# Kernel optimization log

Measured on AMD Instinct MI355X. Metric: run time of the kernel, lower is better.

The kernel has to match this reference:

```python
import jax, jax.numpy as jnp
import numpy as np

N, C, T, V, E = 4, 64, 64, 1024, 4096
IN_CH, OUT_CH, H = 256, 512, 8
DH = OUT_CH // H


def _leaky(x):
    return jnp.where(x >= 0, x, 0.01 * x)


def _mlp(x, w1, b1, w2, b2, g, b):
    # Linear -> LeakyReLU -> (dropout: eval identity) -> Linear -> BatchNorm(batch stats) -> LeakyReLU
    h = _leaky(x @ w1 + b1)
    h = h @ w2 + b2
    n, e, f = h.shape
    flat = h.reshape(n * e, f)
    mu = flat.mean(0)
    var = flat.var(0)  # biased variance, as torch BatchNorm uses for normalization
    flat = (flat - mu) * jax.lax.rsqrt(var + 1e-5) * g + b
    return _leaky(flat.reshape(n, e, f))


def _attn(q, k, v, wq, bq, wk, bk, wv, bv, wf, bf):
    # SelfAttention with scale=1: embed dim == OUT_CH, H heads of DH dims
    n, lq, _ = q.shape
    def split(t):
        return t.reshape(n, -1, H, DH).transpose(0, 2, 1, 3)  # (n, H, L, DH)
    Q = split(q @ wq + bq)
    K = split(k @ wk + bk)
    Vv = split(v @ wv + bv)
    scale = jnp.sqrt(jnp.float32(DH))
    att = jax.nn.softmax(jnp.einsum("nhqd,nhkd->nhqk", Q, K) / scale, axis=-1)
    x = jnp.einsum("nhqk,nhkd->nhqd", att, Vv)
    x = x.transpose(0, 2, 1, 3).reshape(n, lq, OUT_CH)
    return x @ wf + bf


def setup_inputs():
    key = jax.random.key(0)
    ks = list(jax.random.split(key, 24))

    def lin(k1, n_in, n_out):
        w = jax.random.normal(k1, (n_in, n_out), jnp.float32) * np.sqrt(2.0 / (n_in + n_out))
        b = jnp.full((n_out,), 0.1, jnp.float32)
        return w, b

    inp = {
        "x1": jax.random.normal(ks[0], (N, C, T, V), jnp.float32),
        "x2": jax.random.normal(ks[1], (N, C, T, V), jnp.float32),
        "encode1": jax.random.uniform(ks[2], (E, V), dtype=jnp.float32),
        "encode2": jax.random.uniform(ks[3], (E, V), dtype=jnp.float32),
    }
    i = 4
    for name in ("mlp", "nlp"):
        inp[name + "_w1"], inp[name + "_b1"] = lin(ks[i], 2 * IN_CH, OUT_CH); i += 1
        inp[name + "_w2"], inp[name + "_b2"] = lin(ks[i], OUT_CH, OUT_CH); i += 1
        inp[name + "_gamma"] = jnp.ones((OUT_CH,), jnp.float32)
        inp[name + "_beta"] = jnp.zeros((OUT_CH,), jnp.float32)
    for name in ("att1", "att2"):
        for p in ("wq", "wk", "wv", "fc"):
            inp[name + "_" + p + "_w"], inp[name + "_" + p + "_b"] = lin(ks[i], OUT_CH, OUT_CH); i += 1
    return inp


def reference(x1, x2, encode1, encode2,
              mlp_w1, mlp_b1, mlp_w2, mlp_b2, mlp_gamma, mlp_beta,
              nlp_w1, nlp_b1, nlp_w2, nlp_b2, nlp_gamma, nlp_beta,
              att1_wq_w, att1_wq_b, att1_wk_w, att1_wk_b, att1_wv_w, att1_wv_b, att1_fc_w, att1_fc_b,
              att2_wq_w, att2_wq_b, att2_wk_w, att2_wk_b, att2_wv_w, att2_wv_b, att2_fc_w, att2_fc_b):
    n, c, t, v = x1.shape

    def prep(x):
        # permute(0,2,3,1).view(N,V,-1) then AdaptiveAvgPool1d(IN_CH) with exact windows
        x = jnp.transpose(x, (0, 2, 3, 1)).reshape(n, v, t * c)
        return x.reshape(n, v, IN_CH, (t * c) // IN_CH).mean(-1)

    x1p = prep(x1)
    x2p = prep(x2)

    def node_enc(x):
        return jnp.concatenate([
            jnp.einsum("ev,nvc->nec", encode1, x),
            jnp.einsum("ev,nvc->nec", encode2, x),
        ], axis=-1)  # (N, E, 2*IN_CH)

    h1 = _mlp(node_enc(x1p), mlp_w1, mlp_b1, mlp_w2, mlp_b2, mlp_gamma, mlp_beta)
    h2 = _mlp(node_enc(x2p), nlp_w1, nlp_b1, nlp_w2, nlp_b2, nlp_gamma, nlp_beta)

    def edge_enc(h):
        r = jnp.einsum("ev,nec->nvc", encode1, h)  # (N, V, OUT_CH)
        return r / r.shape[1]

    e1 = edge_enc(h1)
    e2 = edge_enc(h2)

    a1 = _attn(e2, e1, e1, att1_wq_w, att1_wq_b, att1_wk_w, att1_wk_b, att1_wv_w, att1_wv_b, att1_fc_w, att1_fc_b)
    a2 = _attn(e1, e2, e2, att2_wq_w, att2_wq_b, att2_wk_w, att2_wk_b, att2_wv_w, att2_wv_b, att2_fc_w, att2_fc_b)

    c1 = jnp.concatenate([a1, a2], axis=1)  # (N, 2V, OUT_CH)
    c2 = jnp.concatenate([a2, a1], axis=1)
    A = jax.nn.softmax(jnp.einsum("nic,njc->nij", c1, c2), axis=-1)  # (N, 2V, 2V)
    # normalize_dynamic_digraph: AGCN-style column-degree normalization A @ D^{-1}
    col = A.sum(axis=1, keepdims=True)
    return A * jnp.where(col > 0, 1.0 / col, 0.0)
```

## Files before the change

### kernel.cpp

```cpp
#include <hip/hip_runtime.h>
#include <hip/hip_bf16.h>

#define LEAKY(v) ((v) >= 0.f ? (v) : 0.01f * (v))

typedef __attribute__((ext_vector_type(8))) short short8b;
typedef __attribute__((ext_vector_type(4))) float f32x4;
typedef __attribute__((ext_vector_type(4))) unsigned short us4;

__device__ __forceinline__ unsigned short f2b(float f) {
  unsigned int u = __builtin_bit_cast(unsigned int, f);
  return (unsigned short)((u + 0x7FFFu + ((u >> 16) & 1u)) >> 16);
}
__device__ __forceinline__ float b2f(unsigned short s) {
  return __builtin_bit_cast(float, (unsigned int)s << 16);
}

__device__ __forceinline__ void gload16(const unsigned short* g, unsigned short* l) {
  __builtin_amdgcn_global_load_lds(
      (const __attribute__((address_space(1))) unsigned int*)(g),
      (__attribute__((address_space(3))) unsigned int*)(l), 16, 0, 0);
}

__device__ __forceinline__ void stage64(const unsigned short* g, int ldg,
                                        unsigned short* lds, int lane, int w) {
  const int r8 = lane >> 3;
  const int ce = ((lane & 7) ^ r8) << 3;
  const int r0 = w * 8 + r8;
  gload16(g + (long)r0 * ldg + ce, lds + w * 512);
  gload16(g + (long)(r0 + 32) * ldg + ce, lds + 2048 + w * 512);
}

__device__ __forceinline__ short8b ldsw(const unsigned short* base, int row, int c4) {
  return *(const short8b*)&base[row * 64 + (((c4 ^ (row & 7)) << 3))];
}

__global__ __launch_bounds__(256) void prep_pool(const float* __restrict__ X1,
                                                 const float* __restrict__ X2,
                                                 unsigned short* __restrict__ P) {
  const float* X = blockIdx.z ? X2 : X1;
  unsigned short* Pb = P + (long)blockIdx.z * (1L << 20);
  const int i = blockIdx.x, n = blockIdx.y;
  const int t = i >> 4;
  const int vvb = (i & 15) * 64;
  __shared__ float tile[64][65];
  const int tid = threadIdx.x;
  const long base = (((long)n * 64) * 64 + t) * 1024 + vvb;
#pragma unroll
  for (int it = 0; it < 16; ++it) {
    int idx = tid + it * 256;
    int c = idx >> 6, w = idx & 63;
    tile[c][w] = X[base + (long)c * 64 * 1024 + w];
  }
  __syncthreads();
  const int k = tid;
  const int w = k >> 2, cb = (k & 3) * 16;
  float s = 0.f;
#pragma unroll
  for (int m = 0; m < 16; ++m) s += tile[cb + m][w];
  Pb[((long)n * 1024 + i) * 256 + k] = f2b(s * (1.f / 16.f));
}

__global__ __launch_bounds__(256) void transpose_f2b(
    const float* __restrict__ in, unsigned short* __restrict__ out, int R, int C) {
  __shared__ float t[64][65];
  const int c0 = blockIdx.x * 64, r0 = blockIdx.y * 64;
  const int tid = threadIdx.x;
#pragma unroll
  for (int it = 0; it < 4; ++it) {
    int idx = tid + it * 256;
    int r = idx >> 4, c4 = (idx & 15) * 4;
    float4 v = *(const float4*)&in[(long)(r0 + r) * C + c0 + c4];
    t[c4 + 0][r] = v.x; t[c4 + 1][r] = v.y;
    t[c4 + 2][r] = v.z; t[c4 + 3][r] = v.w;
  }
  __syncthreads();
#pragma unroll
  for (int it = 0; it < 4; ++it) {
    int idx = tid + it * 256;
    int c = idx >> 4, r4 = (idx & 15) * 4;
    us4 o;
    o[0] = f2b(t[c][r4 + 0]); o[1] = f2b(t[c][r4 + 1]);
    o[2] = f2b(t[c][r4 + 2]); o[3] = f2b(t[c][r4 + 3]);
    *(us4*)&out[(long)(c0 + c) * R + r0 + r4] = o;
  }
}

struct WPtrs { const float* p[12]; };
__global__ __launch_bounds__(256) void wtrans(WPtrs wp, unsigned short* __restrict__ out) {
  const float* in = wp.p[blockIdx.z];
  unsigned short* ob = out + (long)blockIdx.z * 262144;
  __shared__ float t[64][65];
  const int c0 = blockIdx.x * 64, r0 = blockIdx.y * 64;
  const int tid = threadIdx.x;
#pragma unroll
  for (int it = 0; it < 4; ++it) {
    int idx = tid + it * 256;
    int r = idx >> 4, c4 = (idx & 15) * 4;
    float4 v = *(const float4*)&in[(long)(r0 + r) * 512 + c0 + c4];
    t[c4 + 0][r] = v.x; t[c4 + 1][r] = v.y;
    t[c4 + 2][r] = v.z; t[c4 + 3][r] = v.w;
  }
  __syncthreads();
#pragma unroll
  for (int it = 0; it < 4; ++it) {
    int idx = tid + it * 256;
    int c = idx >> 4, r4 = (idx & 15) * 4;
    us4 o;
    o[0] = f2b(t[c][r4 + 0]); o[1] = f2b(t[c][r4 + 1]);
    o[2] = f2b(t[c][r4 + 2]); o[3] = f2b(t[c][r4 + 3]);
    *(us4*)&ob[(long)(c0 + c) * 512 + r0 + r4] = o;
  }
}

__global__ __launch_bounds__(256) void transpose_b2b(
    const unsigned short* __restrict__ in, unsigned short* __restrict__ out,
    int R, int C, long sIn, long sOut) {
  const unsigned short* ib = in + (long)blockIdx.z * sIn;
  unsigned short* ob = out + (long)blockIdx.z * sOut;
  __shared__ unsigned short t[64][65];
  const int c0 = blockIdx.x * 64, r0 = blockIdx.y * 64;
  const int tid = threadIdx.x;
#pragma unroll
  for (int it = 0; it < 2; ++it) {
    int idx = tid + it * 256;
    int r = idx >> 3, c8 = (idx & 7) * 8;
    short8b v = *(const short8b*)&ib[(long)(r0 + r) * C + c0 + c8];
#pragma unroll
    for (int j = 0; j < 8; ++j) t[c8 + j][r] = (unsigned short)v[j];
  }
  __syncthreads();
#pragma unroll
  for (int it = 0; it < 4; ++it) {
    int idx = tid + it * 256;
    int c = idx >> 4, r4 = (idx & 15) * 4;
    us4 o;
    o[0] = t[c][r4 + 0]; o[1] = t[c][r4 + 1];
    o[2] = t[c][r4 + 2]; o[3] = t[c][r4 + 3];
    *(us4*)&ob[(long)(c0 + c) * R + r0 + r4] = o;
  }
}

__global__ __launch_bounds__(256) void convert2_f2b(const float* __restrict__ i1,
                                                    const float* __restrict__ i2,
                                                    unsigned short* __restrict__ out) {
  const float* in = blockIdx.z ? i2 : i1;
  unsigned short* o = out + (long)blockIdx.z * (4L << 20);
  long i = (long)blockIdx.x * 256 + threadIdx.x;
  float4 v = ((const float4*)in)[i];
  us4 q;
  q[0] = f2b(v.x); q[1] = f2b(v.y); q[2] = f2b(v.z); q[3] = f2b(v.w);
  ((us4*)o)[i] = q;
}

__global__ __launch_bounds__(256) void addcvt(const float* __restrict__ P0,
                                              const float* __restrict__ P1,
                                              unsigned short* __restrict__ out,
                                              float alpha) {
  const long i = ((long)blockIdx.x * 256 + threadIdx.x) * 4;
  const float4 a = *(const float4*)&P0[i];
  const float4 b = *(const float4*)&P1[i];
  us4 o;
  o[0] = f2b((a.x + b.x) * alpha);
  o[1] = f2b((a.y + b.y) * alpha);
  o[2] = f2b((a.z + b.z) * alpha);
  o[3] = f2b((a.w + b.w) * alpha);
  *(us4*)&out[i] = o;
}

struct GDesc { const unsigned short* A; const unsigned short* B; long coff; const float* bias; };
struct GDescs { GDesc d[16]; };

template <int ACT, int CMODE, int KSPLIT>
__global__ __launch_bounds__(256) void gemm_z(
    GDescs ga, void* __restrict__ Cv, int K, int lda, int ldb, int ldc,
    long sC2, float alpha) {
  const int bz = blockIdx.z;
  const int s = (KSPLIT > 1) ? (bz % KSPLIT) : 0;
  const int zb = (KSPLIT > 1) ? (bz / KSPLIT) : bz;
  const GDesc g = ga.d[zb];
  const unsigned short* Ab = g.A + (long)s * K;
  const unsigned short* Bb = g.B + (long)s * K;
  const int m0 = blockIdx.y * 128, n0 = blockIdx.x * 128;
  const int tid = threadIdx.x;
  const int lane = tid & 63, w = tid >> 6;
  const int wr = (w >> 1) * 64, wc = (w & 1) * 64;
  __shared__ unsigned short As[128 * 64];
  __shared__ unsigned short Bs[128 * 64];
  f32x4 acc[4][4];
#pragma unroll
  for (int i = 0; i < 4; ++i)
#pragma unroll
    for (int j = 0; j < 4; ++j) acc[i][j] = (f32x4){0.f, 0.f, 0.f, 0.f};
  const int srow = tid >> 3;
  const int scol = (((tid & 7) ^ ((tid >> 3) & 7)) << 3);
  const int rl = lane & 15, lg = lane >> 4, rx = rl & 7;
  for (int k0 = 0; k0 < K; k0 += 64) {
    __syncthreads();
#pragma unroll
    for (int it = 0; it < 4; ++it) {
      gload16(Ab + (long)(m0 + it * 32 + srow) * lda + k0 + scol,
              As + w * 512 + it * 2048);
      gload16(Bb + (long)(n0 + it * 32 + srow) * ldb + k0 + scol,
              Bs + w * 512 + it * 2048);
    }
    __syncthreads();
#pragma unroll
    for (int kk = 0; kk < 2; ++kk) {
      short8b af[4], bfr[4];
#pragma unroll
      for (int m = 0; m < 4; ++m)
        af[m] = *(const short8b*)&As[(wr + m * 16 + rl) * 64 +
                                     ((((kk * 4 + lg) ^ rx)) << 3)];
#pragma unroll
      for (int nn = 0; nn < 4; ++nn)
        bfr[nn] = *(const short8b*)&Bs[(wc + nn * 16 + rl) * 64 +
                                       ((((kk * 4 + lg) ^ rx)) << 3)];
#pragma unroll
      for (int m = 0; m < 4; ++m)
#pragma unroll
        for (int nn = 0; nn < 4; ++nn)
          acc[m][nn] = __builtin_amdgcn_mfma_f32_16x16x32_bf16(
              af[m], bfr[nn], acc[m][nn], 0, 0, 0);
    }
  }
  const int rrow = lg * 4;
  float bv[4];
#pragma unroll
  for (int nn = 0; nn < 4; ++nn)
    bv[nn] = g.bias ? g.bias[n0 + wc + nn * 16 + rl] : 0.f;
  if (CMODE == 2) {
#pragma unroll
    for (int m = 0; m < 4; ++m)
#pragma unroll
      for (int nn = 0; nn < 4; ++nn) {
        const int row = m0 + wr + m * 16 + rrow;
        const int col = n0 + wc + nn * 16 + rl;
        us4 o;
#pragma unroll
        for (int r = 0; r < 4; ++r) {
          float v = alpha * acc[m][nn][r] + bv[nn];
          if (ACT == 1) v = LEAKY(v);
          o[r] = f2b(v);
        }
        const long off = g.coff + (long)(row >> 10) * 524288 +
                         (long)col * 1024 + (row & 1023);
        *(us4*)&((unsigned short*)Cv)[off] = o;
      }
  } else if (CMODE == 3) {
#pragma unroll
    for (int m = 0; m < 4; ++m)
#pragma unroll
      for (int nn = 0; nn < 4; ++nn) {
        const int row = m0 + wr + m * 16 + rrow;
        const int col = n0 + wc + nn * 16 + rl;
        us4 o;
#pragma unroll
        for (int r = 0; r < 4; ++r) {
          float v = alpha * acc[m][nn][r] + bv[nn];
          if (ACT == 1) v = LEAKY(v);
          o[r] = f2b(v);
        }
        *(us4*)&((unsigned short*)Cv)[g.coff + (long)col * ldc + row] = o;
      }
  } else {
#pragma unroll
    for (int m = 0; m < 4; ++m)
#pragma unroll
      for (int nn = 0; nn < 4; ++nn)
#pragma unroll
        for (int r = 0; r < 4; ++r) {
          float v = alpha * acc[m][nn][r] + bv[nn];
          if (ACT == 1) v = LEAKY(v);
          long off = g.coff + (long)s * sC2 +
                     (long)(m0 + wr + m * 16 + rrow + r) * ldc + n0 + wc +
                     nn * 16 + rl;
          if (CMODE == 1)
            ((unsigned short*)Cv)[off] = f2b(v);
          else
            ((float*)Cv)[off] = v;
        }
  }
}

__global__ __launch_bounds__(256) void bn_stats_t(const unsigned short* __restrict__ X,
                                                  float* __restrict__ ST) {
  const int f = blockIdx.x;
  const unsigned short* p = X + (long)f * 16384;
  const int tid = threadIdx.x;
  float s = 0.f, q = 0.f;
#pragma unroll
  for (int k = 0; k < 16; ++k) {
    us4 v = *(const us4*)&p[(k * 256 + tid) * 4];
#pragma unroll
    for (int j = 0; j < 4; ++j) {
      const float x = b2f(v[j]);
      s += x; q += x * x;
    }
  }
#pragma unroll
  for (int mask = 1; mask < 64; mask <<= 1) {
    s += __shfl_xor(s, mask, 64);
    q += __shfl_xor(q, mask, 64);
  }
  __shared__ float rs[8];
  const int wv = tid >> 6;
  if ((tid & 63) == 0) { rs[wv] = s; rs[4 + wv] = q; }
  __syncthreads();
  if (tid == 0) {
    s = rs[0] + rs[1] + rs[2] + rs[3];
    q = rs[4] + rs[5] + rs[6] + rs[7];
    const float mu = s * (1.f / 16384.f);
    ST[f] = mu;
    ST[512 + f] = q * (1.f / 16384.f) - mu * mu;
  }
}

__global__ __launch_bounds__(256) void bn_apply_t(
    unsigned short* __restrict__ X, const float* __restrict__ ST,
    const float* __restrict__ g, const float* __restrict__ be) {
  const long i = ((long)blockIdx.x * 256 + threadIdx.x) * 4;
  const int f = (int)(i >> 14);
  const float rs = rsqrtf(ST[512 + f] + 1e-5f) * g[f];
  const float bb = be[f] - ST[f] * rs;
  us4 v = *(const us4*)&X[i];
  us4 o;
#pragma unroll
  for (int j = 0; j < 4; ++j) {
    const float y = b2f(v[j]) * rs + bb;
    o[j] = f2b(LEAKY(y));
  }
  *(us4*)&X[i] = o;
}

__global__ __launch_bounds__(256) void attn_mfma(
    const unsigned short* __restrict__ Q, const unsigned short* __restrict__ K,
    const unsigned short* __restrict__ Vt, unsigned short* __restrict__ O) {
  const int qb = blockIdx.x, h = blockIdx.y;
  const int n = blockIdx.z & 3, sel = blockIdx.z >> 2;
  Q += (long)sel * 4194304;
  K += (long)sel * 4194304;
  Vt += (long)sel * 2097152;
  O += (long)sel * 2097152;
  const int tid = threadIdx.x;
  const int lane = tid & 63, w = tid >> 6;
  const int rl = lane & 15, lg = lane >> 4;
  __shared__ unsigned short Qs[4096];
  __shared__ unsigned short Ks[4096];
  __shared__ unsigned short Vs[4096];
  __shared__ unsigned short Ps[4096];
  stage64(Q + ((long)n * 1024 + qb * 64) * 512 + h * 64, 512, Qs, lane, w);
  float m_r = -1e30f, l_r = 0.f;
  f32x4 po[4];
#pragma unroll
  for (int i = 0; i < 4; ++i) po[i] = (f32x4){0.f, 0.f, 0.f, 0.f};
  const unsigned short* Kg0 = K + ((long)n * 1024) * 512 + h * 64;
  const unsigned short* Vg0 = Vt + (long)n * 524288 + (long)(h * 64) * 1024;
  for (int kt = 0; kt < 16; ++kt) {
    __syncthreads();
    stage64(Kg0 + (long)(kt * 64) * 512, 512, Ks, lane, w);
    stage64(Vg0 + kt * 64, 1024, Vs, lane, w);
    __syncthreads();
    f32x4 sa[4];
#pragma unroll
    for (int i = 0; i < 4; ++i) sa[i] = (f32x4){0.f, 0.f, 0.f, 0.f};
#pragma unroll
    for (int kk = 0; kk < 2; ++kk) {
      const short8b qf = ldsw(Qs, w * 16 + rl, 4 * kk + lg);
#pragma unroll
      for (int mt = 0; mt < 4; ++mt) {
        const short8b kf = ldsw(Ks, mt * 16 + rl, 4 * kk + lg);
        sa[mt] = __builtin_amdgcn_mfma_f32_16x16x32_bf16(kf, qf, sa[mt], 0, 0, 0);
      }
    }
    float pr[4][4];
    float mx = -1e30f;
#pragma unroll
    for (int mt = 0; mt < 4; ++mt)
#pragma unroll
      for (int r = 0; r < 4; ++r) {
        pr[mt][r] = sa[mt][r] * 0.125f;
        mx = fmaxf(mx, pr[mt][r]);
      }
    mx = fmaxf(mx, __shfl_xor(mx, 16, 64));
    mx = fmaxf(mx, __shfl_xor(mx, 32, 64));
    const float mn = fmaxf(m_r, mx);
    const float f = __expf(m_r - mn);
    m_r = mn;
    float ps = 0.f;
    const int q = w * 16 + rl;
#pragma unroll
    for (int mt = 0; mt < 4; ++mt) {
      us4 o;
#pragma unroll
      for (int r = 0; r < 4; ++r) {
        const float p = __expf(pr[mt][r] - mn);
        ps += p;
        o[r] = f2b(p);
      }
      const int c16 = (4 * mt + lg) >> 1;
      *(us4*)&Ps[q * 64 + ((c16 ^ (q & 7)) << 3) + ((lg & 1) << 2)] = o;
    }
    ps += __shfl_xor(ps, 16, 64);
    ps += __shfl_xor(ps, 32, 64);
    l_r = l_r * f + ps;
#pragma unroll
    for (int r = 0; r < 4; ++r) {
      const float fr = __shfl(f, lg * 4 + r, 64);
#pragma unroll
      for (int nt = 0; nt < 4; ++nt) po[nt][r] *= fr;
    }
#pragma unroll
    for (int kk = 0; kk < 2; ++kk) {
      const short8b pf = ldsw(Ps, w * 16 + rl, 4 * kk + lg);
#pragma unroll
      for (int nt = 0; nt < 4; ++nt) {
        const short8b vf = ldsw(Vs, nt * 16 + rl, 4 * kk + lg);
        po[nt] = __builtin_amdgcn_mfma_f32_16x16x32_bf16(pf, vf, po[nt], 0, 0, 0);
      }
    }
  }
  float invr[4];
#pragma unroll
  for (int r = 0; r < 4; ++r) invr[r] = 1.f / __shfl(l_r, lg * 4 + r, 64);
  const long ob = ((long)n * 1024 + qb * 64 + w * 16) * 512 + h * 64;
#pragma unroll
  for (int nt = 0; nt < 4; ++nt)
#pragma unroll
    for (int r = 0; r < 4; ++r)
      O[ob + (long)(lg * 4 + r) * 512 + nt * 16 + rl] = f2b(po[nt][r] * invr[r]);
}

__global__ __launch_bounds__(256) void softmax_cs(const float* __restrict__ D,
                                                  float* __restrict__ RS,
                                                  float* __restrict__ CS) {
  __shared__ float colacc[2048];
  __shared__ float red[8];
  const int tid = threadIdx.x;
  const int wv = tid >> 6, ln = tid & 63;
#pragma unroll
  for (int k = 0; k < 8; ++k) colacc[tid + k * 256] = 0.f;
  __syncthreads();
  const int r0 = blockIdx.x * 8;
  const int n = r0 >> 11;
  for (int rr = 0; rr < 8; ++rr) {
    const float* p = D + (long)(r0 + rr) * 2048;
    float v[8];
    float mx = -1e30f;
#pragma unroll
    for (int k = 0; k < 8; ++k) {
      v[k] = p[tid + k * 256];
      mx = fmaxf(mx, v[k]);
    }
#pragma unroll
    for (int mask = 1; mask < 64; mask <<= 1) mx = fmaxf(mx, __shfl_xor(mx, mask, 64));
    if (ln == 0) red[wv] = mx;
    __syncthreads();
    mx = fmaxf(fmaxf(red[0], red[1]), fmaxf(red[2], red[3]));
    float sum = 0.f;
#pragma unroll
    for (int k = 0; k < 8; ++k) {
      v[k] = __expf(v[k] - mx);
      sum += v[k];
    }
#pragma unroll
    for (int mask = 1; mask < 64; mask <<= 1) sum += __shfl_xor(sum, mask, 64);
    if (ln == 0) red[4 + wv] = sum;
    __syncthreads();
    sum = red[4] + red[5] + red[6] + red[7];
    const float inv = 1.f / sum;
    if (tid == 0) {
      RS[(r0 + rr) * 2] = mx;
      RS[(r0 + rr) * 2 + 1] = inv;
    }
#pragma unroll
    for (int k = 0; k < 8; ++k) colacc[tid + k * 256] += v[k] * inv;
    __syncthreads();
  }
#pragma unroll
  for (int k = 0; k < 8; ++k)
    atomicAdd(&CS[n * 2048 + tid + k * 256], colacc[tid + k * 256]);
}

__global__ __launch_bounds__(256) void final_scale(float* __restrict__ D,
                                                   const float* __restrict__ RS,
                                                   const float* __restrict__ CS) {
  const long i = ((long)blockIdx.x * 256 + threadIdx.x) * 4;
  const long row = i >> 11;
  const int n = (int)(row >> 11);
  const int j = (int)(i & 2047);
  const float mx = RS[row * 2];
  const float inv = RS[row * 2 + 1];
  float4 v = *(float4*)&D[i];
  const float* c = &CS[n * 2048 + j];
  v.x = __expf(v.x - mx) * inv * (c[0] > 0.f ? 1.f / c[0] : 0.f);
  v.y = __expf(v.y - mx) * inv * (c[1] > 0.f ? 1.f / c[1] : 0.f);
  v.z = __expf(v.z - mx) * inv * (c[2] > 0.f ? 1.f / c[2] : 0.f);
  v.w = __expf(v.w - mx) * inv * (c[3] > 0.f ? 1.f / c[3] : 0.f);
  *(float4*)&D[i] = v;
}

extern "C" void kernel_launch(void* const* d_in, const int* in_sizes, int n_in,
                              void* d_out, int out_size, void* d_ws,
                              size_t ws_size, hipStream_t stream) {
  const float* x1 = (const float*)d_in[0];
  const float* x2 = (const float*)d_in[1];
  const float* enc1 = (const float*)d_in[2];
  const float* enc2 = (const float*)d_in[3];
  const float* mlp_b1 = (const float*)d_in[5];
  const float* mlp_b2 = (const float*)d_in[7];
  const float* mlp_g = (const float*)d_in[8];
  const float* mlp_be = (const float*)d_in[9];
  const float* nlp_b1 = (const float*)d_in[11];
  const float* nlp_b2 = (const float*)d_in[13];
  const float* nlp_g = (const float*)d_in[14];
  const float* nlp_be = (const float*)d_in[15];
  float* out = (float*)d_out;

  unsigned short* W = (unsigned short*)d_ws;
  const long M1 = 1L << 20;
  const long S = 262144;
  unsigned short* Pb1 = W;
  unsigned short* Pt1 = W + 2 * M1;
  unsigned short* E1B = W + 4 * M1;
  unsigned short* E2B = W + 8 * M1;
  unsigned short* E1T = W + 12 * M1;
  unsigned short* WT = W + 16 * M1;
  unsigned short* BA = W + 20 * M1;
  unsigned short* BB = W + 28 * M1;
  unsigned short* H1T = W + 36 * M1;
  unsigned short* H2T = W + 44 * M1;
  unsigned short* E1 = W + 52 * M1;
  float* ST = (float*)(W + 56 * M1);
  float* CS = ST + 1024;
  float* RS = CS + 8192;
  float* P0f = (float*)BA;
  float* P1f = (float*)BB;
  unsigned short* A1P = E2B;
  unsigned short* A2P = E2B + 2 * M1;

  const dim3 T(256);
  const long sP = 262144;
  const long sNE = 2097152;
  const long sE = 524288;
  const long sD = 4194304;

  prep_pool<<<dim3(1024, 4, 2), T, 0, stream>>>(x1, x2, Pb1);
  transpose_b2b<<<dim3(4, 16, 8), T, 0, stream>>>(Pb1, Pt1, 1024, 256, sP, sP);
  convert2_f2b<<<dim3(4096, 1, 2), T, 0, stream>>>(enc1, enc2, E1B);
  transpose_f2b<<<dim3(16, 64), T, 0, stream>>>(enc1, E1T, 4096, 1024);
  WPtrs wp;
  wp.p[0] = (const float*)d_in[4];
  wp.p[1] = (const float*)d_in[6];
  wp.p[2] = (const float*)d_in[10];
  wp.p[3] = (const float*)d_in[12];
  wp.p[4] = (const float*)d_in[16];
  wp.p[5] = (const float*)d_in[18];
  wp.p[6] = (const float*)d_in[24];
  wp.p[7] = (const float*)d_in[26];
  wp.p[8] = (const float*)d_in[20];
  wp.p[9] = (const float*)d_in[28];
  wp.p[10] = (const float*)d_in[22];
  wp.p[11] = (const float*)d_in[30];
  wtrans<<<dim3(8, 8, 12), T, 0, stream>>>(wp, WT);

  {
    GDescs g{};
    for (int pr = 0; pr < 2; ++pr)
      for (int n = 0; n < 4; ++n)
        g.d[pr * 4 + n] = {pr ? E2B : E1B, Pt1 + n * sP,
                           (long)n * sNE + pr * 256, nullptr};
    gemm_z<0, 1, 1><<<dim3(2, 32, 8), T, 0, stream>>>(g, BA, 1024, 1024, 1024,
                                                      512, 0, 1.f);
  }
  {
    GDescs g{};
    g.d[0] = {BA, WT + 0 * S, 0, mlp_b1};
    gemm_z<1, 1, 1><<<dim3(4, 128, 1), T, 0, stream>>>(g, BB, 512, 512, 512,
                                                       512, 0, 1.f);
  }
  {
    GDescs g{};
    g.d[0] = {BB, WT + 1 * S, 0, mlp_b2};
    gemm_z<0, 3, 1><<<dim3(4, 128, 1), T, 0, stream>>>(g, H1T, 512, 512, 512,
                                                       16384, 0, 1.f);
  }
  bn_stats_t<<<512, T, 0, stream>>>(H1T, ST);
  bn_apply_t<<<8192, T, 0, stream>>>(H1T, ST, mlp_g, mlp_be);

  {
    GDescs g{};
    for (int pr = 0; pr < 2; ++pr)
      for (int n = 0; n < 4; ++n)
        g.d[pr * 4 + n] = {pr ? E2B : E1B, Pt1 + M1 + n * sP,
                           (long)n * sNE + pr * 256, nullptr};
    gemm_z<0, 1, 1><<<dim3(2, 32, 8), T, 0, stream>>>(g, BA, 1024, 1024, 1024,
                                                      512, 0, 1.f);
  }
  {
    GDescs g{};
    g.d[0] = {BA, WT + 2 * S, 0, nlp_b1};
    gemm_z<1, 1, 1><<<dim3(4, 128, 1), T, 0, stream>>>(g, BB, 512, 512, 512,
                                                       512, 0, 1.f);
  }
  {
    GDescs g{};
    g.d[0] = {BB, WT + 3 * S, 0, nlp_b2};
    gemm_z<0, 3, 1><<<dim3(4, 128, 1), T, 0, stream>>>(g, H2T, 512, 512, 512,
                                                       16384, 0, 1.f);
  }
  bn_stats_t<<<512, T, 0, stream>>>(H2T, ST);
  bn_apply_t<<<8192, T, 0, stream>>>(H2T, ST, nlp_g, nlp_be);

  {
    GDescs g{};
    for (int d = 0; d < 8; ++d)
      g.d[d] = {E1T, (d >= 4 ? H2T : H1T) + (d & 3) * 4096, (long)d * 524288,
                nullptr};
    gemm_z<0, 0, 2><<<dim3(4, 8, 16), T, 0, stream>>>(g, P0f, 2048, 4096,
                                                      16384, 512, 4194304, 1.f);
  }
  addcvt<<<4096, T, 0, stream>>>(P0f, P1f, E1, 1.f / 1024.f);

  unsigned short* E2 = E1 + 2 * M1;
  {
    GDescs g{};
    g.d[0] = {E2, WT + 4 * S, 0, (const float*)d_in[17]};
    g.d[1] = {E1, WT + 5 * S, 2 * M1, (const float*)d_in[19]};
    g.d[2] = {E1, WT + 6 * S, 4 * M1, (const float*)d_in[25]};
    g.d[3] = {E2, WT + 7 * S, 6 * M1, (const float*)d_in[27]};
    gemm_z<0, 1, 1><<<dim3(4, 32, 4), T, 0, stream>>>(g, BA, 512, 512, 512,
                                                      512, 0, 1.f);
  }
  {
    GDescs g{};
    g.d[0] = {E1, WT + 8 * S, 0, (const float*)d_in[21]};
    g.d[1] = {E2, WT + 9 * S, 2 * M1, (const float*)d_in[29]};
    gemm_z<0, 2, 1><<<dim3(4, 32, 2), T, 0, stream>>>(g, BB, 512, 512, 512,
                                                      512, 0, 1.f);
  }

  attn_mfma<<<dim3(16, 8, 8), T, 0, stream>>>(BA, BA + 2 * M1, BB, BB + 4 * M1);

  {
    GDescs g{};
    g.d[0] = {BB + 4 * M1, WT + 10 * S, 0, (const float*)d_in[23]};
    g.d[1] = {BB + 6 * M1, WT + 11 * S, 2 * M1, (const float*)d_in[31]};
    gemm_z<0, 1, 1><<<dim3(4, 32, 2), T, 0, stream>>>(g, A1P, 512, 512, 512,
                                                      512, 0, 1.f);
  }

  {
    GDescs g{};
    for (int q = 0; q < 4; ++q)
      for (int n = 0; n < 4; ++n) {
        const unsigned short* A = (q < 2 ? A1P : A2P) + n * sE;
        const unsigned short* B = ((q == 0 || q == 2) ? A2P : A1P) + n * sE;
        const long coff =
            (long)n * sD + (q & 1) * 1024 + (long)(q >> 1) * 2097152;
        g.d[q * 4 + n] = {A, B, coff, nullptr};
      }
    gemm_z<0, 0, 1><<<dim3(8, 8, 16), T, 0, stream>>>(g, out, 512, 512, 512,
                                                      2048, 0, 1.f);
  }

  hipMemsetAsync(CS, 0, 8192 * sizeof(float), stream);
  softmax_cs<<<1024, T, 0, stream>>>(out, RS, CS);
  final_scale<<<16384, T, 0, stream>>>(out, RS, CS);
}
```

Measured before the change: 413.0 us.

## Batch both MLP branches per launch and fuse pooling with transpose

Replaces the pool-then-transpose pair with a single kernel that sums over the channel groups and writes the transposed bf16 layout directly, which removes one launch and one intermediate round trip. The two MLP branches (node encoding GEMM, two linears, BN stats and apply) are merged into single launches by using the z grid dimension, which halves the launch count and gives each launch more blocks. The workspace buffers are reorganised so the batched outputs sit contiguously. This adds aliasing risk between buffers that are now reused (E1 overlays ENC, P0f overlays MID and QKV).

```diff
diff --git a/kernel.cpp b/kernel.cpp
--- a/kernel.cpp
+++ b/kernel.cpp
@@ -34,30 +34,31 @@
   return *(const short8b*)&base[row * 64 + (((c4 ^ (row & 7)) << 3))];
 }
 
-__global__ __launch_bounds__(256) void prep_pool(const float* __restrict__ X1,
-                                                 const float* __restrict__ X2,
-                                                 unsigned short* __restrict__ P) {
-  const float* X = blockIdx.z ? X2 : X1;
-  unsigned short* Pb = P + (long)blockIdx.z * (1L << 20);
-  const int i = blockIdx.x, n = blockIdx.y;
-  const int t = i >> 4;
-  const int vvb = (i & 15) * 64;
-  __shared__ float tile[64][65];
+__global__ __launch_bounds__(256) void prep_pool_t(const float* __restrict__ X1,
+                                                   const float* __restrict__ X2,
+                                                   unsigned short* __restrict__ Pt) {
+  const int t = blockIdx.x;
+  const int cbi = blockIdx.y;
+  const int n = blockIdx.z & 3, inp = blockIdx.z >> 2;
+  const float* X = inp ? X2 : X1;
   const int tid = threadIdx.x;
-  const long base = (((long)n * 64) * 64 + t) * 1024 + vvb;
-#pragma unroll
-  for (int it = 0; it < 16; ++it) {
-    int idx = tid + it * 256;
-    int c = idx >> 6, w = idx & 63;
-    tile[c][w] = X[base + (long)c * 64 * 1024 + w];
-  }
+  __shared__ unsigned short sacc[64][20];
+  float acc[4] = {0.f, 0.f, 0.f, 0.f};
+  const long base0 = (((long)n * 64 + cbi * 16) * 64 + t) * 1024 + tid * 4;
+#pragma unroll
+  for (int m = 0; m < 16; ++m) {
+    const float4 v = *(const float4*)&X[base0 + (long)m * 65536];
+    acc[0] += v.x; acc[1] += v.y; acc[2] += v.z; acc[3] += v.w;
+  }
+  const int q = tid & 15, vb = tid >> 4;
+#pragma unroll
+  for (int j = 0; j < 4; ++j)
+    sacc[q * 4 + j][vb] = f2b(acc[j] * (1.f / 16.f));
   __syncthreads();
-  const int k = tid;
-  const int w = k >> 2, cb = (k & 3) * 16;
-  float s = 0.f;
-#pragma unroll
-  for (int m = 0; m < 16; ++m) s += tile[cb + m][w];
-  Pb[((long)n * 1024 + i) * 256 + k] = f2b(s * (1.f / 16.f));
+  const int vvv = tid >> 2, iq = tid & 3;
+  const us4 o = *(const us4*)&sacc[vvv][iq * 4];
+  *(us4*)&Pt[(long)inp * (1L << 20) + (long)n * 262144 +
+             (long)(vvv * 4 + cbi) * 1024 + t * 16 + iq * 4] = o;
 }
 
 __global__ __launch_bounds__(256) void transpose_f2b(
@@ -109,34 +110,6 @@
     o[0] = f2b(t[c][r4 + 0]); o[1] = f2b(t[c][r4 + 1]);
     o[2] = f2b(t[c][r4 + 2]); o[3] = f2b(t[c][r4 + 3]);
     *(us4*)&ob[(long)(c0 + c) * 512 + r0 + r4] = o;
-  }
-}
-
-__global__ __launch_bounds__(256) void transpose_b2b(
-    const unsigned short* __restrict__ in, unsigned short* __restrict__ out,
-    int R, int C, long sIn, long sOut) {
-  const unsigned short* ib = in + (long)blockIdx.z * sIn;
-  unsigned short* ob = out + (long)blockIdx.z * sOut;
-  __shared__ unsigned short t[64][65];
-  const int c0 = blockIdx.x * 64, r0 = blockIdx.y * 64;
-  const int tid = threadIdx.x;
-#pragma unroll
-  for (int it = 0; it < 2; ++it) {
-    int idx = tid + it * 256;
-    int r = idx >> 3, c8 = (idx & 7) * 8;
-    short8b v = *(const short8b*)&ib[(long)(r0 + r) * C + c0 + c8];
-#pragma unroll
-    for (int j = 0; j < 8; ++j) t[c8 + j][r] = (unsigned short)v[j];
-  }
-  __syncthreads();
-#pragma unroll
-  for (int it = 0; it < 4; ++it) {
-    int idx = tid + it * 256;
-    int c = idx >> 4, r4 = (idx & 15) * 4;
-    us4 o;
-    o[0] = t[c][r4 + 0]; o[1] = t[c][r4 + 1];
-    o[2] = t[c][r4 + 2]; o[3] = t[c][r4 + 3];
-    *(us4*)&ob[(long)(c0 + c) * R + r0 + r4] = o;
   }
 }
 
@@ -285,7 +258,9 @@
 __global__ __launch_bounds__(256) void bn_stats_t(const unsigned short* __restrict__ X,
                                                   float* __restrict__ ST) {
   const int f = blockIdx.x;
-  const unsigned short* p = X + (long)f * 16384;
+  const int z = blockIdx.z;
+  const unsigned short* p = X + (long)z * (8L << 20) + (long)f * 16384;
+  float* st = ST + z * 1024;
   const int tid = threadIdx.x;
   float s = 0.f, q = 0.f;
 #pragma unroll
@@ -310,26 +285,32 @@
     s = rs[0] + rs[1] + rs[2] + rs[3];
     q = rs[4] + rs[5] + rs[6] + rs[7];
     const float mu = s * (1.f / 16384.f);
-    ST[f] = mu;
-    ST[512 + f] = q * (1.f / 16384.f) - mu * mu;
+    st[f] = mu;
+    st[512 + f] = q * (1.f / 16384.f) - mu * mu;
   }
 }
 
 __global__ __launch_bounds__(256) void bn_apply_t(
     unsigned short* __restrict__ X, const float* __restrict__ ST,
-    const float* __restrict__ g, const float* __restrict__ be) {
+    const float* __restrict__ g1, const float* __restrict__ be1,
+    const float* __restrict__ g2, const float* __restrict__ be2) {
+  const int z = blockIdx.z;
+  unsigned short* Xb = X + (long)z * (8L << 20);
+  const float* st = ST + z * 1024;
+  const float* g = z ? g2 : g1;
+  const float* be = z ? be2 : be1;
   const long i = ((long)blockIdx.x * 256 + threadIdx.x) * 4;
   const int f = (int)(i >> 14);
-  const float rs = rsqrtf(ST[512 + f] + 1e-5f) * g[f];
-  const float bb = be[f] - ST[f] * rs;
-  us4 v = *(const us4*)&X[i];
+  const float rs = rsqrtf(st[512 + f] + 1e-5f) * g[f];
+  const float bb = be[f] - st[f] * rs;
+  us4 v = *(const us4*)&Xb[i];
   us4 o;
 #pragma unroll
   for (int j = 0; j < 4; ++j) {
     const float y = b2f(v[j]) * rs + bb;
     o[j] = f2b(LEAKY(y));
   }
-  *(us4*)&X[i] = o;
+  *(us4*)&Xb[i] = o;
 }
 
 __global__ __launch_bounds__(256) void attn_mfma(
@@ -519,24 +500,24 @@
   unsigned short* W = (unsigned short*)d_ws;
   const long M1 = 1L << 20;
   const long S = 262144;
-  unsigned short* Pb1 = W;
-  unsigned short* Pt1 = W + 2 * M1;
-  unsigned short* E1B = W + 4 * M1;
-  unsigned short* E2B = W + 8 * M1;
+  unsigned short* Pt = W;
+  unsigned short* ENC = W + 4 * M1;
   unsigned short* E1T = W + 12 * M1;
   unsigned short* WT = W + 16 * M1;
-  unsigned short* BA = W + 20 * M1;
-  unsigned short* BB = W + 28 * M1;
-  unsigned short* H1T = W + 36 * M1;
-  unsigned short* H2T = W + 44 * M1;
-  unsigned short* E1 = W + 52 * M1;
+  unsigned short* NE = W + 20 * M1;
+  unsigned short* H1T = W + 20 * M1;
+  unsigned short* MID = W + 36 * M1;
+  float* P0f = (float*)(W + 36 * M1);
+  unsigned short* E1 = W + 4 * M1;
+  unsigned short* E2 = W + 6 * M1;
+  unsigned short* QKV = W + 36 * M1;
+  unsigned short* VT = W + 44 * M1;
+  unsigned short* AO = W + 48 * M1;
+  unsigned short* A1P = W + 8 * M1;
+  unsigned short* A2P = W + 10 * M1;
   float* ST = (float*)(W + 56 * M1);
-  float* CS = ST + 1024;
+  float* CS = ST + 2048;
   float* RS = CS + 8192;
-  float* P0f = (float*)BA;
-  float* P1f = (float*)BB;
-  unsigned short* A1P = E2B;
-  unsigned short* A2P = E2B + 2 * M1;
 
   const dim3 T(256);
   const long sP = 262144;
@@ -544,9 +525,8 @@
   const long sE = 524288;
   const long sD = 4194304;
 
-  prep_pool<<<dim3(1024, 4, 2), T, 0, stream>>>(x1, x2, Pb1);
-  transpose_b2b<<<dim3(4, 16, 8), T, 0, stream>>>(Pb1, Pt1, 1024, 256, sP, sP);
-  convert2_f2b<<<dim3(4096, 1, 2), T, 0, stream>>>(enc1, enc2, E1B);
+  prep_pool_t<<<dim3(64, 4, 8), T, 0, stream>>>(x1, x2, Pt);
+  convert2_f2b<<<dim3(4096, 1, 2), T, 0, stream>>>(enc1, enc2, ENC);
   transpose_f2b<<<dim3(16, 64), T, 0, stream>>>(enc1, E1T, 4096, 1024);
   WPtrs wp;
   wp.p[0] = (const float*)d_in[4];
@@ -565,86 +545,66 @@
 
   {
     GDescs g{};
-    for (int pr = 0; pr < 2; ++pr)
-      for (int n = 0; n < 4; ++n)
-        g.d[pr * 4 + n] = {pr ? E2B : E1B, Pt1 + n * sP,
-                           (long)n * sNE + pr * 256, nullptr};
-    gemm_z<0, 1, 1><<<dim3(2, 32, 8), T, 0, stream>>>(g, BA, 1024, 1024, 1024,
-                                                      512, 0, 1.f);
-  }
-  {
-    GDescs g{};
-    g.d[0] = {BA, WT + 0 * S, 0, mlp_b1};
-    gemm_z<1, 1, 1><<<dim3(4, 128, 1), T, 0, stream>>>(g, BB, 512, 512, 512,
+    for (int inp = 0; inp < 2; ++inp)
+      for (int pr = 0; pr < 2; ++pr)
+        for (int nn = 0; nn < 4; ++nn)
+          g.d[inp * 8 + pr * 4 + nn] = {
+              ENC + (long)pr * (4 * M1), Pt + (long)inp * M1 + nn * sP,
+              (long)inp * (8 * M1) + (long)nn * sNE + pr * 256, nullptr};
+    gemm_z<0, 1, 1><<<dim3(2, 32, 16), T, 0, stream>>>(g, NE, 1024, 1024,
+                                                       1024, 512, 0, 1.f);
+  }
+  {
+    GDescs g{};
+    g.d[0] = {NE, WT + 0 * S, 0, mlp_b1};
+    g.d[1] = {NE + 8 * M1, WT + 2 * S, 8 * M1, nlp_b1};
+    gemm_z<1, 1, 1><<<dim3(4, 128, 2), T, 0, stream>>>(g, MID, 512, 512, 512,
                                                        512, 0, 1.f);
   }
   {
     GDescs g{};
-    g.d[0] = {BB, WT + 1 * S, 0, mlp_b2};
-    gemm_z<0, 3, 1><<<dim3(4, 128, 1), T, 0, stream>>>(g, H1T, 512, 512, 512,
+    g.d[0] = {MID, WT + 1 * S, 0, mlp_b2};
+    g.d[1] = {MID + 8 * M1, WT + 3 * S, 8 * M1, nlp_b2};
+    gemm_z<0, 3, 1><<<dim3(4, 128, 2), T, 0, stream>>>(g, H1T, 512, 512, 512,
                                                        16384, 0, 1.f);
   }
-  bn_stats_t<<<512, T, 0, stream>>>(H1T, ST);
-  bn_apply_t<<<8192, T, 0, stream>>>(H1T, ST, mlp_g, mlp_be);
-
-  {
-    GDescs g{};
-    for (int pr = 0; pr < 2; ++pr)
-      for (int n = 0; n < 4; ++n)
-        g.d[pr * 4 + n] = {pr ? E2B : E1B, Pt1 + M1 + n * sP,
-                           (long)n * sNE + pr * 256, nullptr};
-    gemm_z<0, 1, 1><<<dim3(2, 32, 8), T, 0, stream>>>(g, BA, 1024, 1024, 1024,
-                                                      512, 0, 1.f);
-  }
-  {
-    GDescs g{};
-    g.d[0] = {BA, WT + 2 * S, 0, nlp_b1};
-    gemm_z<1, 1, 1><<<dim3(4, 128, 1), T, 0, stream>>>(g, BB, 512, 512, 512,
-                                                       512, 0, 1.f);
-  }
-  {
-    GDescs g{};
-    g.d[0] = {BB, WT + 3 * S, 0, nlp_b2};
-    gemm_z<0, 3, 1><<<dim3(4, 128, 1), T, 0, stream>>>(g, H2T, 512, 512, 512,
-                                                       16384, 0, 1.f);
-  }
-  bn_stats_t<<<512, T, 0, stream>>>(H2T, ST);
-  bn_apply_t<<<8192, T, 0, stream>>>(H2T, ST, nlp_g, nlp_be);
+  bn_stats_t<<<dim3(512, 1, 2), T, 0, stream>>>(H1T, ST);
+  bn_apply_t<<<dim3(8192, 1, 2), T, 0, stream>>>(H1T, ST, mlp_g, mlp_be,
+                                                 nlp_g, nlp_be);
 
   {
     GDescs g{};
     for (int d = 0; d < 8; ++d)
-      g.d[d] = {E1T, (d >= 4 ? H2T : H1T) + (d & 3) * 4096, (long)d * 524288,
-                nullptr};
+      g.d[d] = {E1T, H1T + (long)(d >> 2) * (8 * M1) + (d & 3) * 4096,
+                (long)d * 524288, nullptr};
     gemm_z<0, 0, 2><<<dim3(4, 8, 16), T, 0, stream>>>(g, P0f, 2048, 4096,
                                                       16384, 512, 4194304, 1.f);
   }
-  addcvt<<<4096, T, 0, stream>>>(P0f, P1f, E1, 1.f / 1024.f);
-
-  unsigned short* E2 = E1 + 2 * M1;
+  addcvt<<<4096, T, 0, stream>>>(P0f, P0f + 4194304, E1, 1.f / 1024.f);
+
   {
     GDescs g{};
     g.d[0] = {E2, WT + 4 * S, 0, (const float*)d_in[17]};
     g.d[1] = {E1, WT + 5 * S, 2 * M1, (const float*)d_in[19]};
     g.d[2] = {E1, WT + 6 * S, 4 * M1, (const float*)d_in[25]};
     g.d[3] = {E2, WT + 7 * S, 6 * M1, (const float*)d_in[27]};
-    gemm_z<0, 1, 1><<<dim3(4, 32, 4), T, 0, stream>>>(g, BA, 512, 512, 512,
+    gemm_z<0, 1, 1><<<dim3(4, 32, 4), T, 0, stream>>>(g, QKV, 512, 512, 512,
                                                       512, 0, 1.f);
   }
   {
     GDescs g{};
     g.d[0] = {E1, WT + 8 * S, 0, (const float*)d_in[21]};
     g.d[1] = {E2, WT + 9 * S, 2 * M1, (const float*)d_in[29]};
-    gemm_z<0, 2, 1><<<dim3(4, 32, 2), T, 0, stream>>>(g, BB, 512, 512, 512,
+    gemm_z<0, 2, 1><<<dim3(4, 32, 2), T, 0, stream>>>(g, VT, 512, 512, 512,
                                                       512, 0, 1.f);
   }
 
-  attn_mfma<<<dim3(16, 8, 8), T, 0, stream>>>(BA, BA + 2 * M1, BB, BB + 4 * M1);
-
-  {
-    GDescs g{};
-    g.d[0] = {BB + 4 * M1, WT + 10 * S, 0, (const float*)d_in[23]};
-    g.d[1] = {BB + 6 * M1, WT + 11 * S, 2 * M1, (const float*)d_in[31]};
+  attn_mfma<<<dim3(16, 8, 8), T, 0, stream>>>(QKV, QKV + 2 * M1, VT, AO);
+
+  {
+    GDescs g{};
+    g.d[0] = {AO, WT + 10 * S, 0, (const float*)d_in[23]};
+    g.d[1] = {AO + 2 * M1, WT + 11 * S, 2 * M1, (const float*)d_in[31]};
     gemm_z<0, 1, 1><<<dim3(4, 32, 2), T, 0, stream>>>(g, A1P, 512, 512, 512,
                                                       512, 0, 1.f);
   }
```

After: 392.4 us. 5.0% less time.
